# Performance work log

Hardware: AMD Instinct MI355X
Metric: run time of the kernel (lower is better)

Reference implementation:

```python
import jax, jax.numpy as jnp
import numpy as np

WIN = 7       # window_size (square)
SHIFT = 3     # shift_size
HEADS = 4
WS = WIN * WIN  # 49 tokens per window


def _rel_index():
    # Swin relative position index, shape (WS*WS,), static ints
    coords = np.stack(np.meshgrid(np.arange(WIN), np.arange(WIN), indexing='ij'))
    cf = coords.reshape(2, -1)
    rel = (cf[:, :, None] - cf[:, None, :]).transpose(1, 2, 0)  # (WS, WS, 2)
    rel[:, :, 0] += WIN - 1
    rel[:, :, 1] += WIN - 1
    rel[:, :, 0] *= 2 * WIN - 1
    return rel.sum(-1).reshape(-1)

_REL_IDX = jnp.asarray(_rel_index())


def _attn_mask(H, W):
    # shift mask per window, shape (num_windows, WS, WS), static
    m = np.zeros((H, W), np.float32)
    cnt = 0
    for h in ((0, -WIN), (-WIN, -SHIFT), (-SHIFT, None)):
        for w in ((0, -WIN), (-WIN, -SHIFT), (-SHIFT, None)):
            m[h[0]:h[1], w[0]:w[1]] = cnt
            cnt += 1
    m = m.reshape(H // WIN, WIN, W // WIN, WIN).transpose(0, 2, 1, 3).reshape(-1, WS)
    diff = m[:, None, :] - m[:, :, None]
    return np.where(diff == 0, 0.0, -100.0).astype(np.float32)


def setup_inputs() -> dict:
    key = jax.random.key(0)
    ks = jax.random.split(key, 6)
    C = 128
    return {
        'x': jax.random.normal(ks[0], (64, 56, 56, C), jnp.float32),
        'qkv_kernel': jax.random.normal(ks[1], (C, 3 * C), jnp.float32) * (C ** -0.5),
        'qkv_bias': jax.random.normal(ks[2], (3 * C,), jnp.float32) * 0.02,
        'proj_kernel': jax.random.normal(ks[3], (C, C), jnp.float32) * (C ** -0.5),
        'proj_bias': jax.random.normal(ks[4], (C,), jnp.float32) * 0.02,
        'rel_pos_table': jax.random.normal(ks[5], ((2 * WIN - 1) ** 2, HEADS), jnp.float32) * 0.02,
    }


def reference(x, qkv_kernel, qkv_bias, proj_kernel, proj_bias, rel_pos_table):
    B, H, W, C = x.shape
    nH, nW = H // WIN, W // WIN
    head_dim = C // HEADS

    # cyclic shift + window partition -> (B*nH*nW, WS, C)
    xs = jnp.roll(x, (-SHIFT, -SHIFT), axis=(1, 2))
    xw = xs.reshape(B, nH, WIN, nW, WIN, C).transpose(0, 1, 3, 2, 4, 5).reshape(B * nH * nW, WS, C)

    qkv = xw @ qkv_kernel + qkv_bias
    qkv = qkv.reshape(-1, WS, 3, HEADS, head_dim).transpose(2, 0, 3, 1, 4)  # (3, n, h, WS, d)
    q, k, v = qkv[0], qkv[1], qkv[2]

    attn = jnp.einsum('nhsd,nhtd->nhst', q * head_dim ** -0.5, k)

    # relative position bias: (1, heads, WS, WS)
    bias = rel_pos_table[_REL_IDX].reshape(WS, WS, HEADS).transpose(2, 0, 1)[None]
    attn = attn + bias

    # shift mask (static)
    mask = jnp.asarray(_attn_mask(H, W))  # (nH*nW, WS, WS)
    attn = attn.reshape(B, nH * nW, HEADS, WS, WS) + mask[None, :, None]
    attn = jax.nn.softmax(attn.reshape(-1, HEADS, WS, WS), axis=-1)

    out = jnp.einsum('nhst,nhtd->nhsd', attn, v).transpose(0, 2, 1, 3).reshape(-1, WS, C)
    out = out @ proj_kernel + proj_bias

    # window merge + reverse shift
    out = out.reshape(B, nH, nW, WIN, WIN, C).transpose(0, 1, 3, 2, 4, 5).reshape(B, H, W, C)
    return jnp.roll(out, (SHIFT, SHIFT), axis=(1, 2))
```

## Files before the change

### kernel.cpp

```cpp
#include <hip/hip_runtime.h>
#include <hip/hip_bf16.h>

#define WIN 7
#define SHIFT_SZ 3
#define WSQ 49
#define CH 128
#define HW 56
#define LOG2E 1.4426950408889634f
#define QSCALE (0.17677669529663687f * LOG2E)

typedef short s16x8 __attribute__((ext_vector_type(8)));
typedef short s16x4 __attribute__((ext_vector_type(4)));
typedef float f32x4 __attribute__((ext_vector_type(4)));


__global__ void prep_weights(const float* __restrict__ qkv_kernel,
                             const float* __restrict__ proj_kernel,
                             __hip_bfloat16* __restrict__ ws) {
  int idx = blockIdx.x * 256 + threadIdx.x;
  if (idx < 49152) {
    int n = idx >> 7, c = idx & 127;
    ws[idx] = __float2bfloat16(qkv_kernel[c * 384 + n]);
  }
  if (idx < 16384) {
    int n = idx >> 7, c = idx & 127;
    ws[49152 + idx] = __float2bfloat16(proj_kernel[c * 128 + n]);
  }
}

__global__ void prep_tbl(const float* __restrict__ rel_pos_table,
                         __hip_bfloat16* __restrict__ tbl) {
  int idx = blockIdx.x * 256 + threadIdx.x;
  int t = idx & 63;
  int s = (idx >> 6) & 63;
  int h = (idx >> 12) & 3;
  int win = idx >> 14;
  float v;
  if (t >= WSQ) v = -43280.f;
  else if (s >= WSQ) v = 0.f;
  else {
    int i1 = s / 7, j1 = s % 7, i2 = t / 7, j2 = t % 7;
    int ridx = (i1 - i2 + 6) * 13 + (j1 - j2 + 6);
    float bias = rel_pos_table[ridx * 4 + h];
    int wy = win >> 3, wx = win & 7;
    int rh1 = (wy < 7) ? 0 : (i1 < 4 ? 1 : 2);
    int rh2 = (wy < 7) ? 0 : (i2 < 4 ? 1 : 2);
    int rw1 = (wx < 7) ? 0 : (j1 < 4 ? 1 : 2);
    int rw2 = (wx < 7) ? 0 : (j2 < 4 ? 1 : 2);
    float mask = (rh1 == rh2 && rw1 == rw2) ? 0.f : -100.f;
    v = (bias + mask) * LOG2E;
  }
  tbl[idx] = __float2bfloat16(v);
}


static __device__ __forceinline__ s16x8 ld2x64(const __hip_bfloat16* p) {
  s16x8 r;
  *(s16x4*)&r = *(const s16x4*)p;
  *(((s16x4*)&r) + 1) = *(const s16x4*)(p + 4);
  return r;
}

__launch_bounds__(512, 6)
__global__ void swin_attn(const float* __restrict__ x,
                          const float* __restrict__ qkv_bias,
                          const float* __restrict__ proj_bias,
                          const __hip_bfloat16* __restrict__ wqkvT,
                          const __hip_bfloat16* __restrict__ wprojT,
                          const __hip_bfloat16* __restrict__ tbl,
                          float* __restrict__ out) {
  __shared__ __align__(16) char smem[53248];
  __hip_bfloat16* a_lds  = (__hip_bfloat16*)smem;
  __hip_bfloat16* q_lds  = (__hip_bfloat16*)smem;
  __hip_bfloat16* k_lds  = (__hip_bfloat16*)(smem + 18432);
  __hip_bfloat16* vt_lds = (__hip_bfloat16*)(smem + 36864);
  __hip_bfloat16* p_lds  = (__hip_bfloat16*)smem;
  __hip_bfloat16* o_lds  = (__hip_bfloat16*)smem;

  const int tid = threadIdx.x;
  const int lane = tid & 63;
  const int wv = tid >> 6;
  const int g = lane >> 4;
  const int c = lane & 15;

  const int widx = blockIdx.x;
  const int b  = widx >> 6;
  const int wy = (widx >> 3) & 7;
  const int wx = widx & 7;
  const int win64 = widx & 63;

  for (int it = tid; it < 1024; it += 512) {
    int s = it >> 4;
    int l16 = it & 15;
    union { s16x8 v; __hip_bfloat16 h[8]; } u;
    if (s < WSQ) {
      int i = s / 7, j = s - i * 7;
      int hh = wy * 7 + i + SHIFT_SZ; if (hh >= HW) hh -= HW;
      int ww = wx * 7 + j + SHIFT_SZ; if (ww >= HW) ww -= HW;
      const float4* src = (const float4*)(x + (((b * HW + hh) * HW + ww) * CH + l16 * 8));
      float4 f0 = src[0], f1 = src[1];
      u.h[0] = __float2bfloat16(f0.x); u.h[1] = __float2bfloat16(f0.y);
      u.h[2] = __float2bfloat16(f0.z); u.h[3] = __float2bfloat16(f0.w);
      u.h[4] = __float2bfloat16(f1.x); u.h[5] = __float2bfloat16(f1.y);
      u.h[6] = __float2bfloat16(f1.z); u.h[7] = __float2bfloat16(f1.w);
    } else {
      #pragma unroll
      for (int q = 0; q < 8; ++q) u.h[q] = __float2bfloat16(0.f);
    }
    *(s16x8*)(a_lds + s * 136 + l16 * 8) = u.v;
  }
  __syncthreads();

  {
    f32x4 acc_v[4];
    #pragma unroll
    for (int mt = 0; mt < 4; ++mt) acc_v[mt] = (f32x4){0.f, 0.f, 0.f, 0.f};
    #pragma unroll
    for (int kt = 0; kt < 4; ++kt) {
      s16x8 bv = *(const s16x8*)(wqkvT + (16 * (16 + wv) + c) * 128 + kt * 32 + g * 8);
      #pragma unroll
      for (int mt = 0; mt < 4; ++mt) {
        s16x8 af = *(const s16x8*)(a_lds + (16 * mt + c) * 136 + kt * 32 + g * 8);
        acc_v[mt] = __builtin_amdgcn_mfma_f32_16x16x32_bf16(af, bv, acc_v[mt], 0, 0, 0);
      }
    }
    int hv = wv >> 1;
    int d = (wv & 1) * 16 + c;
    float bvb = qkv_bias[256 + wv * 16 + c];
    __hip_bfloat16* vdst = vt_lds + (hv * 32 + d) * 64;
    #pragma unroll
    for (int mt = 0; mt < 4; ++mt) {
      int s0 = 16 * mt + 4 * g;
      union { s16x4 v; __hip_bfloat16 h[4]; } u;
      #pragma unroll
      for (int r = 0; r < 4; ++r) u.h[r] = __float2bfloat16(acc_v[mt][r] + bvb);
      *(s16x4*)(vdst + (((s0 >> 3) ^ (c & 7)) << 3) + (s0 & 7)) = u.v;
    }
  }

  {
    f32x4 acc[2][4];
    #pragma unroll
    for (int ntl = 0; ntl < 2; ++ntl)
      #pragma unroll
      for (int mt = 0; mt < 4; ++mt) acc[ntl][mt] = (f32x4){0.f, 0.f, 0.f, 0.f};
    #pragma unroll
    for (int kt = 0; kt < 4; ++kt) {
      s16x8 af[4];
      #pragma unroll
      for (int mt = 0; mt < 4; ++mt)
        af[mt] = *(const s16x8*)(a_lds + (16 * mt + c) * 136 + kt * 32 + g * 8);
      #pragma unroll
      for (int ntl = 0; ntl < 2; ++ntl) {
        s16x8 bf = *(const s16x8*)(wqkvT + (16 * (2 * wv + ntl) + c) * 128 + kt * 32 + g * 8);
        #pragma unroll
        for (int mt = 0; mt < 4; ++mt)
          acc[ntl][mt] = __builtin_amdgcn_mfma_f32_16x16x32_bf16(bf, af[mt], acc[ntl][mt], 0, 0, 0);
      }
    }
    const float scale = (wv < 4) ? QSCALE : 1.0f;
    if (wv >= 4) {
      #pragma unroll
      for (int ntl = 0; ntl < 2; ++ntl) {
        int qt = 2 * wv + ntl;
        int h = (qt >> 1) & 3;
        int d0 = (qt & 1) * 16 + 4 * g;
        float4 b4 = *(const float4*)(qkv_bias + qt * 16 + 4 * g);
        __hip_bfloat16* dst = k_lds + h * 2304 + d0;
        #pragma unroll
        for (int mt = 0; mt < 4; ++mt) {
          union { s16x4 v; __hip_bfloat16 h[4]; } u;
          u.h[0] = __float2bfloat16((acc[ntl][mt][0] + b4.x) * scale);
          u.h[1] = __float2bfloat16((acc[ntl][mt][1] + b4.y) * scale);
          u.h[2] = __float2bfloat16((acc[ntl][mt][2] + b4.z) * scale);
          u.h[3] = __float2bfloat16((acc[ntl][mt][3] + b4.w) * scale);
          *(s16x4*)(dst + (16 * mt + c) * 36) = u.v;
        }
      }
    }
    __syncthreads();
    if (wv < 4) {
      #pragma unroll
      for (int ntl = 0; ntl < 2; ++ntl) {
        int qt = 2 * wv + ntl;
        int h = (qt >> 1) & 3;
        int d0 = (qt & 1) * 16 + 4 * g;
        float4 b4 = *(const float4*)(qkv_bias + qt * 16 + 4 * g);
        __hip_bfloat16* dst = q_lds + h * 2304 + d0;
        #pragma unroll
        for (int mt = 0; mt < 4; ++mt) {
          union { s16x4 v; __hip_bfloat16 h[4]; } u;
          u.h[0] = __float2bfloat16((acc[ntl][mt][0] + b4.x) * scale);
          u.h[1] = __float2bfloat16((acc[ntl][mt][1] + b4.y) * scale);
          u.h[2] = __float2bfloat16((acc[ntl][mt][2] + b4.z) * scale);
          u.h[3] = __float2bfloat16((acc[ntl][mt][3] + b4.w) * scale);
          *(s16x4*)(dst + (16 * mt + c) * 36) = u.v;
        }
      }
    }
  }
  __syncthreads();

  const int h3 = wv >> 1;
  const int mh = wv & 1;
  s16x8 qf[2], kf[4];
  #pragma unroll
  for (int m = 0; m < 2; ++m)
    qf[m] = ld2x64(q_lds + (h3 * 64 + 16 * (2 * mh + m) + c) * 36 + g * 8);
  #pragma unroll
  for (int nt = 0; nt < 4; ++nt)
    kf[nt] = ld2x64(k_lds + (h3 * 64 + 16 * nt + c) * 36 + g * 8);
  __syncthreads();

  #pragma unroll
  for (int m = 0; m < 2; ++m) {
    f32x4 sc[4];
    #pragma unroll
    for (int nt = 0; nt < 4; ++nt) {
      sc[nt] = (f32x4){0.f, 0.f, 0.f, 0.f};
      sc[nt] = __builtin_amdgcn_mfma_f32_16x16x32_bf16(kf[nt], qf[m], sc[nt], 0, 0, 0);
    }
    const __hip_bfloat16* tb =
        tbl + (((win64 << 2) + h3) << 12) + (16 * (2 * mh + m) + c) * 64;
    #pragma unroll
    for (int nt = 0; nt < 4; ++nt) {
      union { s16x4 v; __hip_bfloat16 h[4]; } tv;
      tv.v = *(const s16x4*)(tb + 16 * nt + 4 * g);
      #pragma unroll
      for (int r = 0; r < 4; ++r) sc[nt][r] += __bfloat162float(tv.h[r]);
    }
    float mx = -1e30f;
    #pragma unroll
    for (int nt = 0; nt < 4; ++nt)
      #pragma unroll
      for (int r = 0; r < 4; ++r) mx = fmaxf(mx, sc[nt][r]);
    mx = fmaxf(mx, __shfl_xor(mx, 16));
    mx = fmaxf(mx, __shfl_xor(mx, 32));
    float sum = 0.f;
    #pragma unroll
    for (int nt = 0; nt < 4; ++nt)
      #pragma unroll
      for (int r = 0; r < 4; ++r) {
        float e = __builtin_amdgcn_exp2f(sc[nt][r] - mx);
        sc[nt][r] = e;
        sum += e;
      }
    sum += __shfl_xor(sum, 16);
    sum += __shfl_xor(sum, 32);
    float inv = __builtin_amdgcn_rcpf(sum);
    __hip_bfloat16* prow = p_lds + (h3 * 64 + 16 * (2 * mh + m) + c) * 72;
    #pragma unroll
    for (int nt = 0; nt < 4; ++nt) {
      union { s16x4 v; __hip_bfloat16 h[4]; } u;
      #pragma unroll
      for (int r = 0; r < 4; ++r) u.h[r] = __float2bfloat16(sc[nt][r] * inv);
      *(s16x4*)(prow + 16 * nt + 4 * g) = u.v;
    }
  }

  f32x4 oacc[2][2];
  #pragma unroll
  for (int m = 0; m < 2; ++m)
    #pragma unroll
    for (int ntd = 0; ntd < 2; ++ntd) oacc[m][ntd] = (f32x4){0.f, 0.f, 0.f, 0.f};
  #pragma unroll
  for (int kt = 0; kt < 2; ++kt) {
    s16x8 vfr[2], pfr[2];
    #pragma unroll
    for (int ntd = 0; ntd < 2; ++ntd)
      vfr[ntd] = *(const s16x8*)(vt_lds + (h3 * 32 + 16 * ntd + c) * 64 +
                                 (((4 * kt + g) ^ (c & 7)) << 3));
    #pragma unroll
    for (int m = 0; m < 2; ++m)
      pfr[m] = *(const s16x8*)(p_lds + (h3 * 64 + 16 * (2 * mh + m) + c) * 72 +
                               kt * 32 + g * 8);
    #pragma unroll
    for (int m = 0; m < 2; ++m)
      #pragma unroll
      for (int ntd = 0; ntd < 2; ++ntd)
        oacc[m][ntd] = __builtin_amdgcn_mfma_f32_16x16x32_bf16(vfr[ntd], pfr[m], oacc[m][ntd], 0, 0, 0);
  }
  __syncthreads();

  #pragma unroll
  for (int m = 0; m < 2; ++m)
    #pragma unroll
    for (int ntd = 0; ntd < 2; ++ntd) {
      union { s16x4 v; __hip_bfloat16 h[4]; } u;
      #pragma unroll
      for (int r = 0; r < 4; ++r) u.h[r] = __float2bfloat16(oacc[m][ntd][r]);
      *(s16x4*)(o_lds + (16 * (2 * mh + m) + c) * 136 + h3 * 32 + 16 * ntd + 4 * g) = u.v;
    }
  __syncthreads();

  {
    f32x4 pacc[4];
    #pragma unroll
    for (int mt = 0; mt < 4; ++mt) pacc[mt] = (f32x4){0.f, 0.f, 0.f, 0.f};
    #pragma unroll
    for (int kt = 0; kt < 4; ++kt) {
      s16x8 bfp = *(const s16x8*)(wprojT + (16 * wv + c) * 128 + kt * 32 + g * 8);
      #pragma unroll
      for (int mt = 0; mt < 4; ++mt) {
        s16x8 afo = *(const s16x8*)(o_lds + (16 * mt + c) * 136 + kt * 32 + g * 8);
        pacc[mt] = __builtin_amdgcn_mfma_f32_16x16x32_bf16(bfp, afo, pacc[mt], 0, 0, 0);
      }
    }
    float4 pb4 = *(const float4*)(proj_bias + 16 * wv + 4 * g);
    #pragma unroll
    for (int mt = 0; mt < 4; ++mt) {
      int s = 16 * mt + c;
      if (s < WSQ) {
        int i = s / 7, j = s - i * 7;
        int hh = wy * 7 + i + SHIFT_SZ; if (hh >= HW) hh -= HW;
        int ww = wx * 7 + j + SHIFT_SZ; if (ww >= HW) ww -= HW;
        float4 v;
        v.x = pacc[mt][0] + pb4.x;
        v.y = pacc[mt][1] + pb4.y;
        v.z = pacc[mt][2] + pb4.z;
        v.w = pacc[mt][3] + pb4.w;
        *(float4*)(out + ((b * HW + hh) * HW + ww) * CH + 16 * wv + 4 * g) = v;
      }
    }
  }
}

extern "C" void kernel_launch(void* const* d_in, const int* in_sizes, int n_in,
                              void* d_out, int out_size, void* d_ws, size_t ws_size,
                              hipStream_t stream) {
  const float* x            = (const float*)d_in[0];
  const float* qkv_kernel   = (const float*)d_in[1];
  const float* qkv_bias     = (const float*)d_in[2];
  const float* proj_kernel  = (const float*)d_in[3];
  const float* proj_bias    = (const float*)d_in[4];
  const float* rel_pos_tbl  = (const float*)d_in[5];
  float* out = (float*)d_out;

  __hip_bfloat16* wsb    = (__hip_bfloat16*)d_ws;
  __hip_bfloat16* wqkvT  = wsb;
  __hip_bfloat16* wprojT = wsb + 49152;
  __hip_bfloat16* tbl    = wsb + 65536;

  prep_weights<<<dim3(192), dim3(256), 0, stream>>>(qkv_kernel, proj_kernel, wsb);
  prep_tbl<<<dim3(4096), dim3(256), 0, stream>>>(rel_pos_tbl, tbl);
  swin_attn<<<dim3(4096), dim3(512), 0, stream>>>(x, qkv_bias, proj_bias,
                                                  wqkvT, wprojT, tbl, out);
}
```

Before: 129.8 us.

## Keep Q, P and V in registers via 16x16x16 MFMA and shrink LDS

Reorganises the per-window attention so Q and the softmax probabilities stay in registers, arranged so their MFMA output layout feeds the next 16x16x16 bf16 MFMA directly, with no round-trip through LDS. V is held in registers and written to LDS only after the A tile is dead. The shared-memory footprint drops from about 52 KB to 35 KB and launch bounds rise to 8 waves per EU to allow more resident blocks. In exchange it uses more registers, issues twice as many half-width MFMAs for QK^T and PV, and each wave recomputes Q for its own rows only.

```diff
diff --git a/kernel.cpp b/kernel.cpp
--- a/kernel.cpp
+++ b/kernel.cpp
@@ -12,6 +12,16 @@
 typedef short s16x8 __attribute__((ext_vector_type(8)));
 typedef short s16x4 __attribute__((ext_vector_type(4)));
 typedef float f32x4 __attribute__((ext_vector_type(4)));
+
+static __device__ __forceinline__ f32x4 mfma16(s16x4 a, s16x4 b, f32x4 c) {
+#if __has_builtin(__builtin_amdgcn_mfma_f32_16x16x16bf16_1k)
+  return __builtin_amdgcn_mfma_f32_16x16x16bf16_1k(a, b, c, 0, 0, 0);
+#else
+  f32x4 d;
+  asm("v_mfma_f32_16x16x16_bf16 %0, %1, %2, %3" : "=v"(d) : "v"(a), "v"(b), "v"(c));
+  return d;
+#endif
+}
 
 
 __global__ void prep_weights(const float* __restrict__ qkv_kernel,
@@ -54,14 +64,7 @@
 }
 
 
-static __device__ __forceinline__ s16x8 ld2x64(const __hip_bfloat16* p) {
-  s16x8 r;
-  *(s16x4*)&r = *(const s16x4*)p;
-  *(((s16x4*)&r) + 1) = *(const s16x4*)(p + 4);
-  return r;
-}
-
-__launch_bounds__(512, 6)
+__launch_bounds__(512, 8)
 __global__ void swin_attn(const float* __restrict__ x,
                           const float* __restrict__ qkv_bias,
                           const float* __restrict__ proj_bias,
@@ -69,13 +72,11 @@
                           const __hip_bfloat16* __restrict__ wprojT,
                           const __hip_bfloat16* __restrict__ tbl,
                           float* __restrict__ out) {
-  __shared__ __align__(16) char smem[53248];
+  __shared__ __align__(16) char smem[35840];
   __hip_bfloat16* a_lds  = (__hip_bfloat16*)smem;
-  __hip_bfloat16* q_lds  = (__hip_bfloat16*)smem;
-  __hip_bfloat16* k_lds  = (__hip_bfloat16*)(smem + 18432);
-  __hip_bfloat16* vt_lds = (__hip_bfloat16*)(smem + 36864);
-  __hip_bfloat16* p_lds  = (__hip_bfloat16*)smem;
-  __hip_bfloat16* o_lds  = (__hip_bfloat16*)smem;
+  __hip_bfloat16* vt_lds = (__hip_bfloat16*)smem;
+  __hip_bfloat16* k_lds  = (__hip_bfloat16*)(smem + 17408);
+  __hip_bfloat16* o_lds  = (__hip_bfloat16*)(smem + 17408);
 
   const int tid = threadIdx.x;
   const int lane = tid & 63;
@@ -88,6 +89,9 @@
   const int wy = (widx >> 3) & 7;
   const int wx = widx & 7;
   const int win64 = widx & 63;
+
+  const int h3 = wv >> 1;
+  const int mh = wv & 1;
 
   for (int it = tid; it < 1024; it += 512) {
     int s = it >> 4;
@@ -112,120 +116,120 @@
   __syncthreads();
 
   {
-    f32x4 acc_v[4];
-    #pragma unroll
-    for (int mt = 0; mt < 4; ++mt) acc_v[mt] = (f32x4){0.f, 0.f, 0.f, 0.f};
+    f32x4 acc[4];
+    #pragma unroll
+    for (int mt = 0; mt < 4; ++mt) acc[mt] = (f32x4){0.f, 0.f, 0.f, 0.f};
+    #pragma unroll
+    for (int kt = 0; kt < 4; ++kt) {
+      s16x8 bf = *(const s16x8*)(wqkvT + (16 * (8 + wv) + c) * 128 + kt * 32 + g * 8);
+      #pragma unroll
+      for (int mt = 0; mt < 4; ++mt) {
+        s16x8 af = *(const s16x8*)(a_lds + (16 * mt + c) * 136 + kt * 32 + g * 8);
+        acc[mt] = __builtin_amdgcn_mfma_f32_16x16x32_bf16(bf, af, acc[mt], 0, 0, 0);
+      }
+    }
+    float4 kb4 = *(const float4*)(qkv_bias + 128 + 16 * wv + 4 * g);
+    __hip_bfloat16* dst = k_lds + (wv >> 1) * 2304 + (wv & 1) * 16 + 4 * g;
+    #pragma unroll
+    for (int mt = 0; mt < 4; ++mt) {
+      union { s16x4 v; __hip_bfloat16 h[4]; } u;
+      u.h[0] = __float2bfloat16(acc[mt][0] + kb4.x);
+      u.h[1] = __float2bfloat16(acc[mt][1] + kb4.y);
+      u.h[2] = __float2bfloat16(acc[mt][2] + kb4.z);
+      u.h[3] = __float2bfloat16(acc[mt][3] + kb4.w);
+      *(s16x4*)(dst + (16 * mt + c) * 36) = u.v;
+    }
+  }
+
+  s16x4 vheld[4];
+  {
+    f32x4 acc[4];
+    #pragma unroll
+    for (int mt = 0; mt < 4; ++mt) acc[mt] = (f32x4){0.f, 0.f, 0.f, 0.f};
     #pragma unroll
     for (int kt = 0; kt < 4; ++kt) {
       s16x8 bv = *(const s16x8*)(wqkvT + (16 * (16 + wv) + c) * 128 + kt * 32 + g * 8);
       #pragma unroll
       for (int mt = 0; mt < 4; ++mt) {
         s16x8 af = *(const s16x8*)(a_lds + (16 * mt + c) * 136 + kt * 32 + g * 8);
-        acc_v[mt] = __builtin_amdgcn_mfma_f32_16x16x32_bf16(af, bv, acc_v[mt], 0, 0, 0);
-      }
-    }
-    int hv = wv >> 1;
-    int d = (wv & 1) * 16 + c;
-    float bvb = qkv_bias[256 + wv * 16 + c];
-    __hip_bfloat16* vdst = vt_lds + (hv * 32 + d) * 64;
+        acc[mt] = __builtin_amdgcn_mfma_f32_16x16x32_bf16(af, bv, acc[mt], 0, 0, 0);
+      }
+    }
+    float vb = qkv_bias[256 + 16 * wv + c];
     #pragma unroll
     for (int mt = 0; mt < 4; ++mt) {
-      int s0 = 16 * mt + 4 * g;
       union { s16x4 v; __hip_bfloat16 h[4]; } u;
       #pragma unroll
-      for (int r = 0; r < 4; ++r) u.h[r] = __float2bfloat16(acc_v[mt][r] + bvb);
-      *(s16x4*)(vdst + (((s0 >> 3) ^ (c & 7)) << 3) + (s0 & 7)) = u.v;
-    }
-  }
-
-  {
-    f32x4 acc[2][4];
+      for (int r = 0; r < 4; ++r) u.h[r] = __float2bfloat16(acc[mt][r] + vb);
+      vheld[mt] = u.v;
+    }
+  }
+
+  s16x4 qf16[2][2];
+  {
+    f32x4 acc[2][2];
     #pragma unroll
     for (int ntl = 0; ntl < 2; ++ntl)
       #pragma unroll
-      for (int mt = 0; mt < 4; ++mt) acc[ntl][mt] = (f32x4){0.f, 0.f, 0.f, 0.f};
+      for (int m = 0; m < 2; ++m) acc[ntl][m] = (f32x4){0.f, 0.f, 0.f, 0.f};
     #pragma unroll
     for (int kt = 0; kt < 4; ++kt) {
-      s16x8 af[4];
-      #pragma unroll
-      for (int mt = 0; mt < 4; ++mt)
-        af[mt] = *(const s16x8*)(a_lds + (16 * mt + c) * 136 + kt * 32 + g * 8);
+      s16x8 afq[2];
+      #pragma unroll
+      for (int m = 0; m < 2; ++m)
+        afq[m] = *(const s16x8*)(a_lds + (16 * (2 * mh + m) + c) * 136 + kt * 32 + g * 8);
       #pragma unroll
       for (int ntl = 0; ntl < 2; ++ntl) {
-        s16x8 bf = *(const s16x8*)(wqkvT + (16 * (2 * wv + ntl) + c) * 128 + kt * 32 + g * 8);
+        s16x8 bf = *(const s16x8*)(wqkvT + (16 * (2 * h3 + ntl) + c) * 128 + kt * 32 + g * 8);
         #pragma unroll
-        for (int mt = 0; mt < 4; ++mt)
-          acc[ntl][mt] = __builtin_amdgcn_mfma_f32_16x16x32_bf16(bf, af[mt], acc[ntl][mt], 0, 0, 0);
-      }
-    }
-    const float scale = (wv < 4) ? QSCALE : 1.0f;
-    if (wv >= 4) {
-      #pragma unroll
-      for (int ntl = 0; ntl < 2; ++ntl) {
-        int qt = 2 * wv + ntl;
-        int h = (qt >> 1) & 3;
-        int d0 = (qt & 1) * 16 + 4 * g;
-        float4 b4 = *(const float4*)(qkv_bias + qt * 16 + 4 * g);
-        __hip_bfloat16* dst = k_lds + h * 2304 + d0;
-        #pragma unroll
-        for (int mt = 0; mt < 4; ++mt) {
-          union { s16x4 v; __hip_bfloat16 h[4]; } u;
-          u.h[0] = __float2bfloat16((acc[ntl][mt][0] + b4.x) * scale);
-          u.h[1] = __float2bfloat16((acc[ntl][mt][1] + b4.y) * scale);
-          u.h[2] = __float2bfloat16((acc[ntl][mt][2] + b4.z) * scale);
-          u.h[3] = __float2bfloat16((acc[ntl][mt][3] + b4.w) * scale);
-          *(s16x4*)(dst + (16 * mt + c) * 36) = u.v;
-        }
-      }
-    }
-    __syncthreads();
-    if (wv < 4) {
-      #pragma unroll
-      for (int ntl = 0; ntl < 2; ++ntl) {
-        int qt = 2 * wv + ntl;
-        int h = (qt >> 1) & 3;
-        int d0 = (qt & 1) * 16 + 4 * g;
-        float4 b4 = *(const float4*)(qkv_bias + qt * 16 + 4 * g);
-        __hip_bfloat16* dst = q_lds + h * 2304 + d0;
-        #pragma unroll
-        for (int mt = 0; mt < 4; ++mt) {
-          union { s16x4 v; __hip_bfloat16 h[4]; } u;
-          u.h[0] = __float2bfloat16((acc[ntl][mt][0] + b4.x) * scale);
-          u.h[1] = __float2bfloat16((acc[ntl][mt][1] + b4.y) * scale);
-          u.h[2] = __float2bfloat16((acc[ntl][mt][2] + b4.z) * scale);
-          u.h[3] = __float2bfloat16((acc[ntl][mt][3] + b4.w) * scale);
-          *(s16x4*)(dst + (16 * mt + c) * 36) = u.v;
-        }
+        for (int m = 0; m < 2; ++m)
+          acc[ntl][m] = __builtin_amdgcn_mfma_f32_16x16x32_bf16(bf, afq[m], acc[ntl][m], 0, 0, 0);
+      }
+    }
+    #pragma unroll
+    for (int ntl = 0; ntl < 2; ++ntl) {
+      float4 qb4 = *(const float4*)(qkv_bias + 32 * h3 + 16 * ntl + 4 * g);
+      #pragma unroll
+      for (int m = 0; m < 2; ++m) {
+        union { s16x4 v; __hip_bfloat16 h[4]; } u;
+        u.h[0] = __float2bfloat16((acc[ntl][m][0] + qb4.x) * QSCALE);
+        u.h[1] = __float2bfloat16((acc[ntl][m][1] + qb4.y) * QSCALE);
+        u.h[2] = __float2bfloat16((acc[ntl][m][2] + qb4.z) * QSCALE);
+        u.h[3] = __float2bfloat16((acc[ntl][m][3] + qb4.w) * QSCALE);
+        qf16[ntl][m] = u.v;
       }
     }
   }
   __syncthreads();
 
-  const int h3 = wv >> 1;
-  const int mh = wv & 1;
-  s16x8 qf[2], kf[4];
-  #pragma unroll
-  for (int m = 0; m < 2; ++m)
-    qf[m] = ld2x64(q_lds + (h3 * 64 + 16 * (2 * mh + m) + c) * 36 + g * 8);
-  #pragma unroll
-  for (int nt = 0; nt < 4; ++nt)
-    kf[nt] = ld2x64(k_lds + (h3 * 64 + 16 * nt + c) * 36 + g * 8);
-  __syncthreads();
-
+  {
+    int row = (wv >> 1) * 32 + (wv & 1) * 16 + c;
+    #pragma unroll
+    for (int mt = 0; mt < 4; ++mt) {
+      int tb = (4 * mt + g) ^ c;
+      *(s16x4*)(vt_lds + row * 64 + tb * 4) = vheld[mt];
+    }
+  }
+
+  s16x4 pf16[2][4];
   #pragma unroll
   for (int m = 0; m < 2; ++m) {
     f32x4 sc[4];
     #pragma unroll
     for (int nt = 0; nt < 4; ++nt) {
       sc[nt] = (f32x4){0.f, 0.f, 0.f, 0.f};
-      sc[nt] = __builtin_amdgcn_mfma_f32_16x16x32_bf16(kf[nt], qf[m], sc[nt], 0, 0, 0);
-    }
-    const __hip_bfloat16* tb =
-        tbl + (((win64 << 2) + h3) << 12) + (16 * (2 * mh + m) + c) * 64;
+      #pragma unroll
+      for (int kb = 0; kb < 2; ++kb) {
+        s16x4 kf = *(const s16x4*)(k_lds + h3 * 2304 + (16 * nt + c) * 36 + 16 * kb + 4 * g);
+        sc[nt] = mfma16(kf, qf16[kb][m], sc[nt]);
+      }
+    }
+    const __hip_bfloat16* tb_ =
+        tbl + (((win64 << 2) + h3) << 12) + (32 * mh + 16 * m + c) * 64;
     #pragma unroll
     for (int nt = 0; nt < 4; ++nt) {
       union { s16x4 v; __hip_bfloat16 h[4]; } tv;
-      tv.v = *(const s16x4*)(tb + 16 * nt + 4 * g);
+      tv.v = *(const s16x4*)(tb_ + 16 * nt + 4 * g);
       #pragma unroll
       for (int r = 0; r < 4; ++r) sc[nt][r] += __bfloat162float(tv.h[r]);
     }
@@ -248,40 +252,34 @@
     sum += __shfl_xor(sum, 16);
     sum += __shfl_xor(sum, 32);
     float inv = __builtin_amdgcn_rcpf(sum);
-    __hip_bfloat16* prow = p_lds + (h3 * 64 + 16 * (2 * mh + m) + c) * 72;
     #pragma unroll
     for (int nt = 0; nt < 4; ++nt) {
       union { s16x4 v; __hip_bfloat16 h[4]; } u;
       #pragma unroll
       for (int r = 0; r < 4; ++r) u.h[r] = __float2bfloat16(sc[nt][r] * inv);
-      *(s16x4*)(prow + 16 * nt + 4 * g) = u.v;
-    }
-  }
+      pf16[m][nt] = u.v;
+    }
+  }
+  __syncthreads();
 
   f32x4 oacc[2][2];
   #pragma unroll
-  for (int m = 0; m < 2; ++m)
-    #pragma unroll
-    for (int ntd = 0; ntd < 2; ++ntd) oacc[m][ntd] = (f32x4){0.f, 0.f, 0.f, 0.f};
-  #pragma unroll
-  for (int kt = 0; kt < 2; ++kt) {
-    s16x8 vfr[2], pfr[2];
-    #pragma unroll
-    for (int ntd = 0; ntd < 2; ++ntd)
-      vfr[ntd] = *(const s16x8*)(vt_lds + (h3 * 32 + 16 * ntd + c) * 64 +
-                                 (((4 * kt + g) ^ (c & 7)) << 3));
-    #pragma unroll
-    for (int m = 0; m < 2; ++m)
-      pfr[m] = *(const s16x8*)(p_lds + (h3 * 64 + 16 * (2 * mh + m) + c) * 72 +
-                               kt * 32 + g * 8);
-    #pragma unroll
-    for (int m = 0; m < 2; ++m)
-      #pragma unroll
-      for (int ntd = 0; ntd < 2; ++ntd)
-        oacc[m][ntd] = __builtin_amdgcn_mfma_f32_16x16x32_bf16(vfr[ntd], pfr[m], oacc[m][ntd], 0, 0, 0);
-  }
-  __syncthreads();
-
+  for (int ntd = 0; ntd < 2; ++ntd) {
+    s16x4 vf16[4];
+    #pragma unroll
+    for (int nt = 0; nt < 4; ++nt) {
+      int row = h3 * 32 + 16 * ntd + c;
+      int tb = (4 * nt + g) ^ c;
+      vf16[nt] = *(const s16x4*)(vt_lds + row * 64 + tb * 4);
+    }
+    #pragma unroll
+    for (int m = 0; m < 2; ++m) {
+      oacc[m][ntd] = (f32x4){0.f, 0.f, 0.f, 0.f};
+      #pragma unroll
+      for (int nt = 0; nt < 4; ++nt)
+        oacc[m][ntd] = mfma16(vf16[nt], pf16[m][nt], oacc[m][ntd]);
+    }
+  }
   #pragma unroll
   for (int m = 0; m < 2; ++m)
     #pragma unroll
@@ -289,7 +287,7 @@
       union { s16x4 v; __hip_bfloat16 h[4]; } u;
       #pragma unroll
       for (int r = 0; r < 4; ++r) u.h[r] = __float2bfloat16(oacc[m][ntd][r]);
-      *(s16x4*)(o_lds + (16 * (2 * mh + m) + c) * 136 + h3 * 32 + 16 * ntd + 4 * g) = u.v;
+      *(s16x4*)(o_lds + (32 * mh + 16 * m + c) * 136 + 32 * h3 + 16 * ntd + 4 * g) = u.v;
     }
   __syncthreads();
 
```

New measurement: 143.7 us. +10.8%, slower.

## Swizzle LDS tiles with XOR layout and shrink bias-mask table to four classes

Applied to the files above, without the earlier changes.

Replaces the padded LDS row strides (136/72) with unpadded 128/64 strides using an XOR swizzle on 16-byte chunks for the activation, P, and O tiles. This avoids bank conflicts without wasting LDS. The O tile moves to the V region so it no longer overlaps P. The precomputed bias+mask table is reduced from 64 windows to 4 mask classes, based on whether the window is on the last row or column. This cuts the prep kernel launch size and the table's global/L2 footprint.

```diff
diff --git a/kernel.cpp b/kernel.cpp
--- a/kernel.cpp
+++ b/kernel.cpp
@@ -34,7 +34,7 @@
   int t = idx & 63;
   int s = (idx >> 6) & 63;
   int h = (idx >> 12) & 3;
-  int win = idx >> 14;
+  int cls = idx >> 14;
   float v;
   if (t >= WSQ) v = -43280.f;
   else if (s >= WSQ) v = 0.f;
@@ -42,11 +42,11 @@
     int i1 = s / 7, j1 = s % 7, i2 = t / 7, j2 = t % 7;
     int ridx = (i1 - i2 + 6) * 13 + (j1 - j2 + 6);
     float bias = rel_pos_table[ridx * 4 + h];
-    int wy = win >> 3, wx = win & 7;
-    int rh1 = (wy < 7) ? 0 : (i1 < 4 ? 1 : 2);
-    int rh2 = (wy < 7) ? 0 : (i2 < 4 ? 1 : 2);
-    int rw1 = (wx < 7) ? 0 : (j1 < 4 ? 1 : 2);
-    int rw2 = (wx < 7) ? 0 : (j2 < 4 ? 1 : 2);
+    int wyIs7 = cls >> 1, wxIs7 = cls & 1;
+    int rh1 = wyIs7 ? (i1 < 4 ? 1 : 2) : 0;
+    int rh2 = wyIs7 ? (i2 < 4 ? 1 : 2) : 0;
+    int rw1 = wxIs7 ? (j1 < 4 ? 1 : 2) : 0;
+    int rw2 = wxIs7 ? (j2 < 4 ? 1 : 2) : 0;
     float mask = (rh1 == rh2 && rw1 == rw2) ? 0.f : -100.f;
     v = (bias + mask) * LOG2E;
   }
@@ -75,19 +75,20 @@
   __hip_bfloat16* k_lds  = (__hip_bfloat16*)(smem + 18432);
   __hip_bfloat16* vt_lds = (__hip_bfloat16*)(smem + 36864);
   __hip_bfloat16* p_lds  = (__hip_bfloat16*)smem;
-  __hip_bfloat16* o_lds  = (__hip_bfloat16*)smem;
+  __hip_bfloat16* o_lds  = (__hip_bfloat16*)(smem + 36864);
 
   const int tid = threadIdx.x;
   const int lane = tid & 63;
   const int wv = tid >> 6;
   const int g = lane >> 4;
   const int c = lane & 15;
+  const int e = c & 7;
 
   const int widx = blockIdx.x;
   const int b  = widx >> 6;
   const int wy = (widx >> 3) & 7;
   const int wx = widx & 7;
-  const int win64 = widx & 63;
+  const int mc = ((wy == 7) ? 2 : 0) + ((wx == 7) ? 1 : 0);
 
   for (int it = tid; it < 1024; it += 512) {
     int s = it >> 4;
@@ -107,7 +108,7 @@
       #pragma unroll
       for (int q = 0; q < 8; ++q) u.h[q] = __float2bfloat16(0.f);
     }
-    *(s16x8*)(a_lds + s * 136 + l16 * 8) = u.v;
+    *(s16x8*)(a_lds + s * 128 + ((l16 ^ (s & 7)) * 8)) = u.v;
   }
   __syncthreads();
 
@@ -120,7 +121,7 @@
       s16x8 bv = *(const s16x8*)(wqkvT + (16 * (16 + wv) + c) * 128 + kt * 32 + g * 8);
       #pragma unroll
       for (int mt = 0; mt < 4; ++mt) {
-        s16x8 af = *(const s16x8*)(a_lds + (16 * mt + c) * 136 + kt * 32 + g * 8);
+        s16x8 af = *(const s16x8*)(a_lds + (16 * mt + c) * 128 + ((4 * kt + g) ^ e) * 8);
         acc_v[mt] = __builtin_amdgcn_mfma_f32_16x16x32_bf16(af, bv, acc_v[mt], 0, 0, 0);
       }
     }
@@ -130,11 +131,10 @@
     __hip_bfloat16* vdst = vt_lds + (hv * 32 + d) * 64;
     #pragma unroll
     for (int mt = 0; mt < 4; ++mt) {
-      int s0 = 16 * mt + 4 * g;
       union { s16x4 v; __hip_bfloat16 h[4]; } u;
       #pragma unroll
       for (int r = 0; r < 4; ++r) u.h[r] = __float2bfloat16(acc_v[mt][r] + bvb);
-      *(s16x4*)(vdst + (((s0 >> 3) ^ (c & 7)) << 3) + (s0 & 7)) = u.v;
+      *(s16x4*)(vdst + ((2 * mt + (g >> 1)) ^ e) * 8 + (g & 1) * 4) = u.v;
     }
   }
 
@@ -149,7 +149,7 @@
       s16x8 af[4];
       #pragma unroll
       for (int mt = 0; mt < 4; ++mt)
-        af[mt] = *(const s16x8*)(a_lds + (16 * mt + c) * 136 + kt * 32 + g * 8);
+        af[mt] = *(const s16x8*)(a_lds + (16 * mt + c) * 128 + ((4 * kt + g) ^ e) * 8);
       #pragma unroll
       for (int ntl = 0; ntl < 2; ++ntl) {
         s16x8 bf = *(const s16x8*)(wqkvT + (16 * (2 * wv + ntl) + c) * 128 + kt * 32 + g * 8);
@@ -220,12 +220,12 @@
       sc[nt] = (f32x4){0.f, 0.f, 0.f, 0.f};
       sc[nt] = __builtin_amdgcn_mfma_f32_16x16x32_bf16(kf[nt], qf[m], sc[nt], 0, 0, 0);
     }
-    const __hip_bfloat16* tb =
-        tbl + (((win64 << 2) + h3) << 12) + (16 * (2 * mh + m) + c) * 64;
+    const __hip_bfloat16* tb_ =
+        tbl + (((mc << 2) + h3) << 12) + (32 * mh + 16 * m + c) * 64;
     #pragma unroll
     for (int nt = 0; nt < 4; ++nt) {
       union { s16x4 v; __hip_bfloat16 h[4]; } tv;
-      tv.v = *(const s16x4*)(tb + 16 * nt + 4 * g);
+      tv.v = *(const s16x4*)(tb_ + 16 * nt + 4 * g);
       #pragma unroll
       for (int r = 0; r < 4; ++r) sc[nt][r] += __bfloat162float(tv.h[r]);
     }
@@ -241,20 +241,20 @@
     for (int nt = 0; nt < 4; ++nt)
       #pragma unroll
       for (int r = 0; r < 4; ++r) {
-        float e = __builtin_amdgcn_exp2f(sc[nt][r] - mx);
-        sc[nt][r] = e;
-        sum += e;
+        float e2 = __builtin_amdgcn_exp2f(sc[nt][r] - mx);
+        sc[nt][r] = e2;
+        sum += e2;
       }
     sum += __shfl_xor(sum, 16);
     sum += __shfl_xor(sum, 32);
     float inv = __builtin_amdgcn_rcpf(sum);
-    __hip_bfloat16* prow = p_lds + (h3 * 64 + 16 * (2 * mh + m) + c) * 72;
+    __hip_bfloat16* prow = p_lds + (h3 * 64 + 16 * (2 * mh + m) + c) * 64;
     #pragma unroll
     for (int nt = 0; nt < 4; ++nt) {
       union { s16x4 v; __hip_bfloat16 h[4]; } u;
       #pragma unroll
       for (int r = 0; r < 4; ++r) u.h[r] = __float2bfloat16(sc[nt][r] * inv);
-      *(s16x4*)(prow + 16 * nt + 4 * g) = u.v;
+      *(s16x4*)(prow + ((2 * nt + (g >> 1)) ^ e) * 8 + (g & 1) * 4) = u.v;
     }
   }
 
@@ -269,11 +269,11 @@
     #pragma unroll
     for (int ntd = 0; ntd < 2; ++ntd)
       vfr[ntd] = *(const s16x8*)(vt_lds + (h3 * 32 + 16 * ntd + c) * 64 +
-                                 (((4 * kt + g) ^ (c & 7)) << 3));
+                                 (((4 * kt + g) ^ e) * 8));
     #pragma unroll
     for (int m = 0; m < 2; ++m)
-      pfr[m] = *(const s16x8*)(p_lds + (h3 * 64 + 16 * (2 * mh + m) + c) * 72 +
-                               kt * 32 + g * 8);
+      pfr[m] = *(const s16x8*)(p_lds + (h3 * 64 + 16 * (2 * mh + m) + c) * 64 +
+                               (((4 * kt + g) ^ e) * 8));
     #pragma unroll
     for (int m = 0; m < 2; ++m)
       #pragma unroll
@@ -289,7 +289,8 @@
       union { s16x4 v; __hip_bfloat16 h[4]; } u;
       #pragma unroll
       for (int r = 0; r < 4; ++r) u.h[r] = __float2bfloat16(oacc[m][ntd][r]);
-      *(s16x4*)(o_lds + (16 * (2 * mh + m) + c) * 136 + h3 * 32 + 16 * ntd + 4 * g) = u.v;
+      *(s16x4*)(o_lds + (32 * mh + 16 * m + c) * 128 +
+                ((4 * h3 + 2 * ntd + (g >> 1)) ^ e) * 8 + (g & 1) * 4) = u.v;
     }
   __syncthreads();
 
@@ -302,7 +303,7 @@
       s16x8 bfp = *(const s16x8*)(wprojT + (16 * wv + c) * 128 + kt * 32 + g * 8);
       #pragma unroll
       for (int mt = 0; mt < 4; ++mt) {
-        s16x8 afo = *(const s16x8*)(o_lds + (16 * mt + c) * 136 + kt * 32 + g * 8);
+        s16x8 afo = *(const s16x8*)(o_lds + (16 * mt + c) * 128 + ((4 * kt + g) ^ e) * 8);
         pacc[mt] = __builtin_amdgcn_mfma_f32_16x16x32_bf16(bfp, afo, pacc[mt], 0, 0, 0);
       }
     }
@@ -342,7 +343,7 @@
   __hip_bfloat16* tbl    = wsb + 65536;
 
   prep_weights<<<dim3(192), dim3(256), 0, stream>>>(qkv_kernel, proj_kernel, wsb);
-  prep_tbl<<<dim3(4096), dim3(256), 0, stream>>>(rel_pos_tbl, tbl);
+  prep_tbl<<<dim3(256), dim3(256), 0, stream>>>(rel_pos_tbl, tbl);
   swin_attn<<<dim3(4096), dim3(512), 0, stream>>>(x, qkv_bias, proj_bias,
                                                   wqkvT, wprojT, tbl, out);
 }
```

After: 126.8 us. 1.02x faster.
